# Performance work log

Measured on AMD Instinct MI355X. Metric: run time of the kernel, lower is better.

Reference implementation:

```python
import jax, jax.numpy as jnp
import numpy as np

NUM_NODES = 16384   # batch_size * nodes_per_query_graph
NODES_PER_GRAPH = 8
NUM_EDGES = 14336   # ~7 edges per query graph
NUM_RELS = 64
DIM = 128
BATCH = NUM_NODES // NODES_PER_GRAPH  # 2048
NUM_PASSES = 2
EPS = 1e-8


def setup_inputs() -> dict:
    key = jax.random.key(0)
    ks = jax.random.split(key, 7)
    x = jax.random.normal(ks[0], (NUM_NODES, DIM), jnp.float32)
    basis = jax.random.normal(ks[1], (NUM_RELS, DIM, DIM), jnp.float32) * 0.05
    root = jax.random.normal(ks[2], (DIM, DIM), jnp.float32) * 0.05
    bias = jax.random.normal(ks[3], (DIM,), jnp.float32) * 0.05
    target_embeds = jax.random.normal(ks[4], (BATCH, DIM), jnp.float32)
    # edges stay within each query graph: pick local src/dst per graph
    graph_of_edge = jnp.repeat(jnp.arange(BATCH), NUM_EDGES // BATCH)
    local = jax.random.randint(ks[5], (2, NUM_EDGES), 0, NODES_PER_GRAPH)
    edge_index = graph_of_edge[None, :] * NODES_PER_GRAPH + local  # [2, E]
    edge_type = jax.random.randint(ks[6], (NUM_EDGES,), 0, NUM_RELS)
    batch_idx = jnp.arange(NUM_NODES) // NODES_PER_GRAPH  # node -> query graph id
    return {"x": x, "basis": basis, "root": root, "bias": bias,
            "target_embeds": target_embeds, "edge_index": edge_index,
            "edge_type": edge_type, "batch_idx": batch_idx}


def rgcn_conv(h, edge_index, edge_type, basis, root, bias):
    # RGCNConv forward (num_bases=0, 'add' aggregation, no edge_norm)
    src, dst = edge_index[0], edge_index[1]
    w = basis[edge_type]                      # [E, D, D] relation-indexed gather
    msg = jnp.einsum('ed,edo->eo', h[src], w)  # per-edge bmm
    aggr = jax.ops.segment_sum(msg, dst, num_segments=h.shape[0])  # scatter-add
    return aggr + h @ root + bias


def reference(x, basis, root, bias, target_embeds, edge_index, edge_type, batch_idx):
    h = x
    for _ in range(NUM_PASSES - 1):
        h = jax.nn.relu(rgcn_conv(h, edge_index, edge_type, basis, root, bias))
    # sum readout per query graph (dropout=0 -> h2 == h1)
    pooled = jax.ops.segment_sum(h, batch_idx, num_segments=target_embeds.shape[0])
    # F.cosine_similarity(out, target_embeds, dim=1)
    num = jnp.sum(pooled * target_embeds, axis=1)
    na = jnp.maximum(jnp.linalg.norm(pooled, axis=1), EPS)
    nb = jnp.maximum(jnp.linalg.norm(target_embeds, axis=1), EPS)
    return num / (na * nb)
```

## Files before the change

### kernel.cpp

```cpp
#include <hip/hip_runtime.h>

#define NUM_NODES 16384
#define NPG 8
#define NUM_EDGES 14336
#define EPG 7
#define NUM_RELS 64
#define DIM 128
#define BATCH 2048
#define EPS 1e-8f

#define SEG 1792
#define EDGE_BLOCKS 512
#define ROOT_BLOCKS 256

using f16x8 = __attribute__((ext_vector_type(8))) _Float16;
using f32x4 = __attribute__((ext_vector_type(4))) float;

#define MSG_OFF 0u
#define RTP_OFF 3670016u
#define WS_NEEDED 7864320u

__global__ __launch_bounds__(256) void gemm2_kernel(
    const float* __restrict__ x, const float* __restrict__ basis,
    const float* __restrict__ root, const int* __restrict__ edge_index,
    const int* __restrict__ edge_type,
    _Float16* __restrict__ msg_h, _Float16* __restrict__ rootp_h)
{
    __shared__ _Float16 Bl[DIM * DIM];
    __shared__ int smeta[128];
    __shared__ int wcnt[4];

    const int bid = blockIdx.x;
    const int tid = threadIdx.x;
    const int lane = tid & 63;
    const int w    = tid >> 6;
    const bool isEdge = bid < EDGE_BLOCKS;

    const float* Bsrc;

    if (isEdge) {
        const int rel  = bid >> 3;
        const int part = bid & 7;
        Bsrc = basis + ((size_t)rel << 14);

        if (tid < 64) { smeta[tid] = 0; smeta[64 + tid] = -1; }
        __syncthreads();

        const int seg0 = part * SEG;
        int run = 0;
        for (int it = 0; it < 7; ++it) {
            const int e = seg0 + it * 256 + tid;
            const bool match = (edge_type[e] == rel);
            const unsigned long long mb = __ballot(match);
            if (lane == 0) wcnt[w] = (int)__popcll(mb);
            __syncthreads();
            int pre = run;
            #pragma unroll
            for (int w2 = 0; w2 < 4; ++w2) if (w2 < w) pre += wcnt[w2];
            const int tot = wcnt[0] + wcnt[1] + wcnt[2] + wcnt[3];
            if (match) {
                const int ord = pre + (int)__popcll(mb & ((1ull << lane) - 1ull));
                if (ord < 64) {
                    smeta[ord] = edge_index[e];
                    smeta[64 + ord] = e;
                }
            }
            run += tot;
            __syncthreads();
        }
        if (run == 0) return;
    } else {
        const int row0 = (bid - EDGE_BLOCKS) * 64;
        Bsrc = root;
        if (tid < 64) {
            smeta[tid] = row0 + tid;
            smeta[64 + tid] = row0 + tid;
        }
    }

    {
        const int br = tid >> 4;
        const int bc = tid & 15;
        const float* src = Bsrc + (br * 8) * DIM + bc * 8;
        _Float16 m[8][8];
        #pragma unroll
        for (int u = 0; u < 8; ++u) {
            const float4 a = *(const float4*)(src + u * DIM);
            const float4 b = *(const float4*)(src + u * DIM + 4);
            m[u][0] = (_Float16)a.x; m[u][1] = (_Float16)a.y;
            m[u][2] = (_Float16)a.z; m[u][3] = (_Float16)a.w;
            m[u][4] = (_Float16)b.x; m[u][5] = (_Float16)b.y;
            m[u][6] = (_Float16)b.z; m[u][7] = (_Float16)b.w;
        }
        #pragma unroll
        for (int c2 = 0; c2 < 8; ++c2) {
            const int col = bc * 8 + c2;
            const int chunk = col * 16 + br;
            const int cs = chunk ^ (c2 & 7) ^ (bc & 7);
            f16x8 v = {m[0][c2], m[1][c2], m[2][c2], m[3][c2],
                       m[4][c2], m[5][c2], m[6][c2], m[7][c2]};
            *(f16x8*)(&Bl[cs * 8]) = v;
        }
    }
    __syncthreads();

    const int l15 = lane & 15;
    const int q   = lane >> 4;

    const int src = smeta[w * 16 + l15];
    const float* xrow = x + ((size_t)src << 7) + q * 8;
    f16x8 a[4];
    #pragma unroll
    for (int kb = 0; kb < 4; ++kb) {
        const float4 lo = *(const float4*)(xrow + kb * 32);
        const float4 hi = *(const float4*)(xrow + kb * 32 + 4);
        f16x8 av;
        av[0] = (_Float16)lo.x; av[1] = (_Float16)lo.y;
        av[2] = (_Float16)lo.z; av[3] = (_Float16)lo.w;
        av[4] = (_Float16)hi.x; av[5] = (_Float16)hi.y;
        av[6] = (_Float16)hi.z; av[7] = (_Float16)hi.w;
        a[kb] = av;
    }

    f32x4 acc[8];
    #pragma unroll
    for (int ct = 0; ct < 8; ++ct) acc[ct] = (f32x4){0.f, 0.f, 0.f, 0.f};

    #pragma unroll
    for (int ct = 0; ct < 8; ++ct) {
        const int col = ct * 16 + l15;
        const int sw  = (col & 7) ^ ((col >> 3) & 7);
        #pragma unroll
        for (int kb = 0; kb < 4; ++kb) {
            const int chunk = col * 16 + kb * 4 + q;
            const int cs = chunk ^ sw;
            const f16x8 bfr = *(const f16x8*)(&Bl[cs * 8]);
            acc[ct] = __builtin_amdgcn_mfma_f32_16x16x32_f16(a[kb], bfr, acc[ct], 0, 0, 0);
        }
    }

    _Float16* outb = isEdge ? msg_h : rootp_h;
    #pragma unroll
    for (int j = 0; j < 4; ++j) {
        const int r = w * 16 + q * 4 + j;
        const int oid = smeta[64 + r];
        if (oid >= 0) {
            #pragma unroll
            for (int ct = 0; ct < 8; ++ct) {
                outb[((size_t)oid << 7) + ct * 16 + l15] = (_Float16)acc[ct][j];
            }
        }
    }
}

__global__ __launch_bounds__(256) void finalize_kernel(
    const _Float16* __restrict__ rootp_h, const _Float16* __restrict__ msg_h,
    const float* __restrict__ bias, const float* __restrict__ target,
    const int* __restrict__ edge_index, float* __restrict__ out)
{
    const int g = blockIdx.x * 4 + (threadIdx.x >> 6);
    const int l = threadIdx.x & 63;
    const int d0 = l * 2;

    const float2 bv = *(const float2*)(bias + d0);
    float accA[NPG], accB[NPG];
    #pragma unroll
    for (int n = 0; n < NPG; ++n) {
        const _Float16* row = rootp_h + ((size_t)(g * NPG + n) << 7) + d0;
        accA[n] = bv.x + (float)row[0];
        accB[n] = bv.y + (float)row[1];
    }

    const int ebase = g * EPG;
    #pragma unroll
    for (int e = 0; e < EPG; ++e) {
        const int ge  = ebase + e;
        const int dst = edge_index[NUM_EDGES + ge] - g * NPG;
        const _Float16* mrow = msg_h + ((size_t)ge << 7) + d0;
        const float m0 = (float)mrow[0];
        const float m1 = (float)mrow[1];
        #pragma unroll
        for (int n = 0; n < NPG; ++n) {
            accA[n] += (n == dst) ? m0 : 0.f;
            accB[n] += (n == dst) ? m1 : 0.f;
        }
    }

    float p0 = 0.f, p1 = 0.f;
    #pragma unroll
    for (int n = 0; n < NPG; ++n) {
        p0 += fmaxf(accA[n], 0.f);
        p1 += fmaxf(accB[n], 0.f);
    }

    const float2 tv = *(const float2*)(target + (size_t)g * DIM + d0);
    float num_p = p0 * tv.x + p1 * tv.y;
    float na_p  = p0 * p0 + p1 * p1;
    float nb_p  = tv.x * tv.x + tv.y * tv.y;

    #pragma unroll
    for (int off = 32; off > 0; off >>= 1) {
        num_p += __shfl_down(num_p, off);
        na_p  += __shfl_down(na_p, off);
        nb_p  += __shfl_down(nb_p, off);
    }
    if (l == 0) {
        const float na = fmaxf(sqrtf(na_p), EPS);
        const float nb = fmaxf(sqrtf(nb_p), EPS);
        out[g] = num_p / (na * nb);
    }
}

__global__ __launch_bounds__(128) void rgcn_fused_kernel(
    const float* __restrict__ x, const float* __restrict__ basis,
    const float* __restrict__ root, const float* __restrict__ bias,
    const float* __restrict__ target, const int* __restrict__ edge_index,
    const int* __restrict__ edge_type, float* __restrict__ out)
{
    const int g = blockIdx.x;
    const int o = threadIdx.x;
    __shared__ float xs[NPG][DIM];
    __shared__ float red[6];
    {
        const float4* xg = reinterpret_cast<const float4*>(x + (size_t)g * NPG * DIM);
        float4* xs4 = reinterpret_cast<float4*>(&xs[0][0]);
        xs4[o] = xg[o];
        xs4[o + 128] = xg[o + 128];
    }
    __syncthreads();
    float acc[NPG];
    const float b = bias[o];
    #pragma unroll
    for (int n = 0; n < NPG; ++n) acc[n] = b;
    for (int d4 = 0; d4 < DIM / 4; ++d4) {
        const float r0 = root[(d4 * 4 + 0) * DIM + o];
        const float r1 = root[(d4 * 4 + 1) * DIM + o];
        const float r2 = root[(d4 * 4 + 2) * DIM + o];
        const float r3 = root[(d4 * 4 + 3) * DIM + o];
        #pragma unroll
        for (int n = 0; n < NPG; ++n) {
            const float4 xv = reinterpret_cast<const float4*>(&xs[n][0])[d4];
            acc[n] += xv.x * r0 + xv.y * r1 + xv.z * r2 + xv.w * r3;
        }
    }
    const int ebase = g * EPG;
    for (int e = 0; e < EPG; ++e) {
        const int ge  = ebase + e;
        const int src = edge_index[ge] - g * NPG;
        const int dst = edge_index[NUM_EDGES + ge] - g * NPG;
        const int rel = edge_type[ge];
        const float* __restrict__ B = basis + (size_t)rel * DIM * DIM;
        float m = 0.f;
        for (int d4 = 0; d4 < DIM / 4; ++d4) {
            const float4 xv = reinterpret_cast<const float4*>(&xs[src][0])[d4];
            m += xv.x * B[(d4 * 4 + 0) * DIM + o];
            m += xv.y * B[(d4 * 4 + 1) * DIM + o];
            m += xv.z * B[(d4 * 4 + 2) * DIM + o];
            m += xv.w * B[(d4 * 4 + 3) * DIM + o];
        }
        #pragma unroll
        for (int n = 0; n < NPG; ++n) acc[n] += (n == dst) ? m : 0.f;
    }
    float p = 0.f;
    #pragma unroll
    for (int n = 0; n < NPG; ++n) p += fmaxf(acc[n], 0.f);
    const float t = target[(size_t)g * DIM + o];
    float num_p = p * t, na_p = p * p, nb_p = t * t;
    #pragma unroll
    for (int off = 32; off > 0; off >>= 1) {
        num_p += __shfl_down(num_p, off);
        na_p  += __shfl_down(na_p, off);
        nb_p  += __shfl_down(nb_p, off);
    }
    const int wave = o >> 6, lane = o & 63;
    if (lane == 0) {
        red[wave * 3 + 0] = num_p;
        red[wave * 3 + 1] = na_p;
        red[wave * 3 + 2] = nb_p;
    }
    __syncthreads();
    if (o == 0) {
        const float num = red[0] + red[3];
        const float na  = fmaxf(sqrtf(red[1] + red[4]), EPS);
        const float nb  = fmaxf(sqrtf(red[2] + red[5]), EPS);
        out[g] = num / (na * nb);
    }
}

extern "C" void kernel_launch(void* const* d_in, const int* in_sizes, int n_in,
                              void* d_out, int out_size, void* d_ws, size_t ws_size,
                              hipStream_t stream) {
    const float* x          = (const float*)d_in[0];
    const float* basis      = (const float*)d_in[1];
    const float* root       = (const float*)d_in[2];
    const float* bias       = (const float*)d_in[3];
    const float* target     = (const float*)d_in[4];
    const int*   edge_index = (const int*)d_in[5];
    const int*   edge_type  = (const int*)d_in[6];
    float* out = (float*)d_out;

    if (ws_size < WS_NEEDED) {
        rgcn_fused_kernel<<<BATCH, 128, 0, stream>>>(
            x, basis, root, bias, target, edge_index, edge_type, out);
        return;
    }

    char* ws = (char*)d_ws;
    _Float16* msg_h   = (_Float16*)(ws + MSG_OFF);
    _Float16* rootp_h = (_Float16*)(ws + RTP_OFF);

    gemm2_kernel<<<EDGE_BLOCKS + ROOT_BLOCKS, 256, 0, stream>>>(
        x, basis, root, edge_index, edge_type, msg_h, rootp_h);
    finalize_kernel<<<BATCH / 4, 256, 0, stream>>>(
        rootp_h, msg_h, bias, target, edge_index, out);
}
```

Before: 23.36 us.

## Replace ballot-scan edge bucketing with shared atomics and reorder root blocks first

Edge-bucketing in the GEMM kernel drops the per-iteration ballot/prefix scan and its two barriers per step. Each matching thread now claims a slot with a shared-memory atomicAdd, and the early exit is deferred until after the basis tile has been staged to LDS. Root blocks are placed first in the grid. The finalize kernel now handles 8 graphs per 512-thread block. Edge order within a relation becomes nondeterministic, and empty-relation blocks still pay for the basis load before they exit.

```diff
diff --git a/kernel.cpp b/kernel.cpp
--- a/kernel.cpp
+++ b/kernel.cpp
@@ -10,8 +10,8 @@
 #define EPS 1e-8f
 
 #define SEG 1792
+#define ROOT_BLOCKS 256
 #define EDGE_BLOCKS 512
-#define ROOT_BLOCKS 256
 
 using f16x8 = __attribute__((ext_vector_type(8))) _Float16;
 using f32x4 = __attribute__((ext_vector_type(4))) float;
@@ -28,53 +28,44 @@
 {
     __shared__ _Float16 Bl[DIM * DIM];
     __shared__ int smeta[128];
-    __shared__ int wcnt[4];
+    __shared__ int lcnt;
 
     const int bid = blockIdx.x;
     const int tid = threadIdx.x;
     const int lane = tid & 63;
     const int w    = tid >> 6;
-    const bool isEdge = bid < EDGE_BLOCKS;
+    const bool isEdge = bid >= ROOT_BLOCKS;
 
     const float* Bsrc;
 
     if (isEdge) {
-        const int rel  = bid >> 3;
-        const int part = bid & 7;
-        Bsrc = basis + ((size_t)rel << 14);
-
         if (tid < 64) { smeta[tid] = 0; smeta[64 + tid] = -1; }
-        __syncthreads();
-
-        const int seg0 = part * SEG;
-        int run = 0;
-        for (int it = 0; it < 7; ++it) {
-            const int e = seg0 + it * 256 + tid;
-            const bool match = (edge_type[e] == rel);
-            const unsigned long long mb = __ballot(match);
-            if (lane == 0) wcnt[w] = (int)__popcll(mb);
-            __syncthreads();
-            int pre = run;
-            #pragma unroll
-            for (int w2 = 0; w2 < 4; ++w2) if (w2 < w) pre += wcnt[w2];
-            const int tot = wcnt[0] + wcnt[1] + wcnt[2] + wcnt[3];
-            if (match) {
-                const int ord = pre + (int)__popcll(mb & ((1ull << lane) - 1ull));
-                if (ord < 64) {
-                    smeta[ord] = edge_index[e];
-                    smeta[64 + ord] = e;
-                }
-            }
-            run += tot;
-            __syncthreads();
-        }
-        if (run == 0) return;
+        if (tid == 0) lcnt = 0;
+        Bsrc = basis + ((size_t)((bid - ROOT_BLOCKS) >> 3) << 14);
     } else {
-        const int row0 = (bid - EDGE_BLOCKS) * 64;
-        Bsrc = root;
+        const int row0 = bid * 64;
         if (tid < 64) {
             smeta[tid] = row0 + tid;
             smeta[64 + tid] = row0 + tid;
+        }
+        Bsrc = root;
+    }
+    __syncthreads();
+
+    if (isEdge) {
+        const int eb   = bid - ROOT_BLOCKS;
+        const int rel  = eb >> 3;
+        const int seg0 = (eb & 7) * SEG;
+        #pragma unroll
+        for (int it = 0; it < 7; ++it) {
+            const int e = seg0 + it * 256 + tid;
+            if (edge_type[e] == rel) {
+                const int pos = atomicAdd(&lcnt, 1);
+                if (pos < 64) {
+                    smeta[pos] = edge_index[e];
+                    smeta[64 + pos] = e;
+                }
+            }
         }
     }
 
@@ -103,6 +94,8 @@
         }
     }
     __syncthreads();
+
+    if (isEdge && lcnt == 0) return;
 
     const int l15 = lane & 15;
     const int q   = lane >> 4;
@@ -153,12 +146,12 @@
     }
 }
 
-__global__ __launch_bounds__(256) void finalize_kernel(
+__global__ __launch_bounds__(512) void finalize_kernel(
     const _Float16* __restrict__ rootp_h, const _Float16* __restrict__ msg_h,
     const float* __restrict__ bias, const float* __restrict__ target,
     const int* __restrict__ edge_index, float* __restrict__ out)
 {
-    const int g = blockIdx.x * 4 + (threadIdx.x >> 6);
+    const int g = blockIdx.x * 8 + (threadIdx.x >> 6);
     const int l = threadIdx.x & 63;
     const int d0 = l * 2;
 
@@ -309,8 +302,8 @@
     _Float16* msg_h   = (_Float16*)(ws + MSG_OFF);
     _Float16* rootp_h = (_Float16*)(ws + RTP_OFF);
 
-    gemm2_kernel<<<EDGE_BLOCKS + ROOT_BLOCKS, 256, 0, stream>>>(
+    gemm2_kernel<<<ROOT_BLOCKS + EDGE_BLOCKS, 256, 0, stream>>>(
         x, basis, root, edge_index, edge_type, msg_h, rootp_h);
-    finalize_kernel<<<BATCH / 4, 256, 0, stream>>>(
+    finalize_kernel<<<BATCH / 8, 512, 0, stream>>>(
         rootp_h, msg_h, bias, target, edge_index, out);
 }
```

New measurement: 22.25 us (median of 2 runs). 4.7% less time.
